# Optimization experiments

Hardware: AMD Instinct MI355X
Metric: run time of the kernel (lower is better)

Reference implementation:

```python
import jax, jax.numpy as jnp
import numpy as np

V, D, B, L = 100000, 64, 4096, 200

def setup_inputs() -> dict:
    key = jax.random.key(0)
    ks = jax.random.split(key, 10)
    s = 0.05  # keep activations in a sane range for sigmoid
    return {
        "item_ids": jax.random.randint(ks[0], (B,), 0, V),
        "history": jax.random.randint(ks[1], (B, L), 0, V),
        "hist_len": jax.random.randint(ks[2], (B,), 1, L + 1),
        "emb_table": jax.random.normal(ks[3], (V, D), jnp.float32) * s,
        "aW1": jax.random.normal(ks[4], (3 * D, D), jnp.float32) * s,
        "ab1": jnp.zeros((D,), jnp.float32),
        "aW2": jax.random.normal(ks[5], (D, 1), jnp.float32) * s,
        "ab2": jnp.zeros((1,), jnp.float32),
        "fW1": jax.random.normal(ks[6], (3 * D, 128), jnp.float32) * s,
        "fb1": jnp.zeros((128,), jnp.float32),
        "fW2": jax.random.normal(ks[7], (128, 64), jnp.float32) * s,
        "fb2": jnp.zeros((64,), jnp.float32),
        "fW3": jax.random.normal(ks[8], (64, 1), jnp.float32) * s,
        "fb3": jnp.zeros((1,), jnp.float32),
    }

def reference(item_ids, history, hist_len, emb_table, aW1, ab1, aW2, ab2,
              fW1, fb1, fW2, fb2, fW3, fb3):
    target = emb_table[item_ids]                      # [B, D]
    hist = emb_table[history]                         # [B, L, D]
    # original pads short histories with zero rows -> zero the padded tail
    mask = (jnp.arange(hist.shape[1])[None, :] < hist_len[:, None]).astype(hist.dtype)
    hist = hist * mask[..., None]
    tgt = jnp.broadcast_to(target[:, None, :], hist.shape)     # [B, L, D]
    # attention_fc takes 3*D features: (hist, target, hist*target)
    feat = jnp.concatenate([hist, tgt, hist * tgt], axis=-1)   # [B, L, 3D]
    h = jax.nn.relu(feat @ aW1 + ab1)                 # [B, L, D]
    scores = (h @ aW2 + ab2)[..., 0]                  # [B, L]
    # faithful to original: softmax over full padded length (no length mask)
    w = jax.nn.softmax(scores, axis=1)
    pooled = jnp.einsum('bl,bld->bd', w, hist)        # [B, D]
    comb = jnp.concatenate([target, pooled, pooled - target], axis=-1)  # [B, 3D]
    z = jax.nn.relu(comb @ fW1 + fb1)
    z = jax.nn.relu(z @ fW2 + fb2)
    return jax.nn.sigmoid(z @ fW3 + fb3)              # [B, 1]
```

## Files before the change

### kernel.cpp

```cpp
#include <hip/hip_runtime.h>
#include <hip/hip_bf16.h>

#define NV 100000
#define ND 64
#define NB 4096
#define NL 200
#define MT 13

typedef __bf16 bf16_t;
typedef __bf16 bf16x8 __attribute__((ext_vector_type(8)));
typedef __bf16 bf16x4 __attribute__((ext_vector_type(4)));
typedef float f32x4 __attribute__((ext_vector_type(4)));

#define TB_ELEMS ((long)NV * ND)
#define TBV (TB_ELEMS / 8)
#define FT1 (128 * 192)
#define FT2 (64 * 128)
#define AWB (192 * 64)
#define CVT_TASKS (TBV + FT1 + FT2 + AWB)

__global__ __launch_bounds__(256)
void cvt_kernel(const float* __restrict__ emb,
                const float* __restrict__ aW1,
                const float* __restrict__ fW1,
                const float* __restrict__ fW2,
                bf16_t* __restrict__ tb,
                bf16_t* __restrict__ fW1T,
                bf16_t* __restrict__ fW2T,
                bf16_t* __restrict__ awB)
{
    long t = (long)blockIdx.x * 256 + threadIdx.x;
    if (t >= CVT_TASKS) return;
    if (t < TBV) {
        long i = t * 8;
        f32x4 a0 = *(const f32x4*)(emb + i);
        f32x4 a1 = *(const f32x4*)(emb + i + 4);
        bf16x8 o;
#pragma unroll
        for (int j = 0; j < 4; ++j) { o[j] = (bf16_t)a0[j]; o[j + 4] = (bf16_t)a1[j]; }
        *(bf16x8*)(tb + i) = o;
    } else {
        int u = (int)(t - TBV);
        if (u < FT1) {
            int n = u / 192, k = u - n * 192;
            fW1T[u] = (bf16_t)fW1[k * 128 + n];
        } else if (u < FT1 + FT2) {
            int u2 = u - FT1;
            int n = u2 >> 7, k = u2 & 127;
            fW2T[u2] = (bf16_t)fW2[k * 64 + n];
        } else {
            int u3 = u - FT1 - FT2;
            awB[u3] = (bf16_t)aW1[u3];
        }
    }
}

__global__ __launch_bounds__(512, 4)
void din_kernel1(const int* __restrict__ item_ids,
                 const int* __restrict__ history,
                 const int* __restrict__ hist_len,
                 const float* __restrict__ emb,
                 const bf16_t* __restrict__ tb,
                 const float* __restrict__ aW1,
                 const bf16_t* __restrict__ awB,
                 const float* __restrict__ ab1,
                 const float* __restrict__ aW2,
                 const bf16_t* __restrict__ fW1T, const float* __restrict__ fb1,
                 const bf16_t* __restrict__ fW2T, const float* __restrict__ fb2,
                 const float* __restrict__ fW3, const float* __restrict__ fb3,
                 float* __restrict__ out)
{
    __shared__ __align__(16) bf16_t histA[2][208 * 64];
    __shared__ __align__(16) bf16_t wbT[2][64 * 64];
    __shared__ float tgt[2][64];
    __shared__ __align__(16) float scores[2][208];
    __shared__ float wts[2][208];
    __shared__ float pp2[2][256];
    __shared__ float red[2][8];
    __shared__ float cb2[2][64];

    bf16_t* comb16 = (bf16_t*)wbT;
    bf16_t* z1s    = (bf16_t*)wbT + 3200;
    float*  z2f    = (float*)((bf16_t*)wbT + 5376);

    const int b0  = blockIdx.x * 2;
    const int tid = threadIdx.x;
    const int len0 = hist_len[b0];
    const int len1 = hist_len[b0 + 1];

    if (tid < 128) {
        int bx = tid >> 6, d = tid & 63;
        tgt[bx][d] = emb[(long)item_ids[b0 + bx] * ND + d];
    }

    {
        const int p = tid & 1;
        const int s = tid >> 1;
        const int bxA = (s >= 208);
        const int lA  = s - bxA * 208;
        const int lB  = s + 48;
        const int lenA = bxA ? len1 : len0;
        const bool vB = (s < 160);
        const bf16x8 z = (bf16x8)(bf16_t)0.f;
        bf16x8 a0 = z, a1 = z, a2 = z, a3 = z;
        bf16x8 c0 = z, c1 = z, c2 = z, c3 = z;
        if (lA < lenA) {
            const bf16_t* src = tb + (long)history[(long)(b0 + bxA) * NL + lA] * ND + p * 32;
            a0 = *(const bf16x8*)(src);
            a1 = *(const bf16x8*)(src + 8);
            a2 = *(const bf16x8*)(src + 16);
            a3 = *(const bf16x8*)(src + 24);
        }
        if (vB && lB < len1) {
            const bf16_t* src = tb + (long)history[(long)(b0 + 1) * NL + lB] * ND + p * 32;
            c0 = *(const bf16x8*)(src);
            c1 = *(const bf16x8*)(src + 8);
            c2 = *(const bf16x8*)(src + 16);
            c3 = *(const bf16x8*)(src + 24);
        }
        {
            bf16_t* d = &histA[bxA][lA * 64];
            const int S = (lA & 7) << 3;
            *(bf16x8*)&d[(p * 32 +  0) ^ S] = a0;
            *(bf16x8*)&d[(p * 32 +  8) ^ S] = a1;
            *(bf16x8*)&d[(p * 32 + 16) ^ S] = a2;
            *(bf16x8*)&d[(p * 32 + 24) ^ S] = a3;
        }
        if (vB) {
            bf16_t* d = &histA[1][lB * 64];
            const int S = (lB & 7) << 3;
            *(bf16x8*)&d[(p * 32 +  0) ^ S] = c0;
            *(bf16x8*)&d[(p * 32 +  8) ^ S] = c1;
            *(bf16x8*)&d[(p * 32 + 16) ^ S] = c2;
            *(bf16x8*)&d[(p * 32 + 24) ^ S] = c3;
        }
    }

    {
        const int lane = tid & 63;
        const int w    = tid >> 6;
        const int bx   = w & 1;
        const int n    = ((w >> 1) << 4) | (lane & 15);
        const int kq   = lane >> 4;
        const long t0  = (long)item_ids[b0 + bx] * ND;
        f32x4 tka = *(const f32x4*)(emb + t0 + kq * 16);
        f32x4 tkb = *(const f32x4*)(emb + t0 + kq * 16 + 4);
        f32x4 tkc = *(const f32x4*)(emb + t0 + kq * 16 + 8);
        f32x4 tkd = *(const f32x4*)(emb + t0 + kq * 16 + 12);
        float csum = 0.f;
        bf16x8 w0v, w1v;
#pragma unroll
        for (int i = 0; i < 16; ++i) {
            int k = kq * 16 + i;
            float tk = (i < 4) ? tka[i] : (i < 8) ? tkb[i - 4]
                     : (i < 12) ? tkc[i - 8] : tkd[i - 12];
            float ah = (float)awB[k * 64 + n];
            float am = aW1[(64 + k) * 64 + n];
            float ap = (float)awB[(128 + k) * 64 + n];
            float wv = ah + tk * ap;
            if (i < 8) w0v[i] = (bf16_t)wv; else w1v[i - 8] = (bf16_t)wv;
            csum += tk * am;
        }
        const int S = (n & 7) << 3;
        *(bf16x8*)&wbT[bx][n * 64 + ((kq * 16    ) ^ S)] = w0v;
        *(bf16x8*)&wbT[bx][n * 64 + ((kq * 16 + 8) ^ S)] = w1v;
        csum += __shfl_xor(csum, 16, 64);
        csum += __shfl_xor(csum, 32, 64);
        if (kq == 0) cb2[bx][n] = ab1[n] + csum;
    }
    __syncthreads();

    {
        const int wave = tid >> 6;
        const int lane = tid & 63;
        const int bx   = wave & 1;
        const int col  = lane & 15;
        const int quad = lane >> 4;

        bf16x8 afrag[4][2];
#pragma unroll
        for (int nt = 0; nt < 4; ++nt) {
            const int n = nt * 16 + col;
            const int S = (n & 7) << 3;
#pragma unroll
            for (int kb = 0; kb < 2; ++kb)
                afrag[nt][kb] = *(const bf16x8*)&wbT[bx][n * 64 + ((kb * 32 + quad * 8) ^ S)];
        }
        float cv[4][4], a2[4][4];
#pragma unroll
        for (int nt = 0; nt < 4; ++nt)
#pragma unroll
            for (int i = 0; i < 4; ++i) {
                const int no = nt * 16 + quad * 4 + i;
                cv[nt][i] = cb2[bx][no];
                a2[nt][i] = aW2[no];
            }

        for (int mt = (wave >> 1); mt < MT; mt += 4) {
            const int l = mt * 16 + col;
            const int S = (l & 7) << 3;
            const bf16_t* base = &histA[bx][l * 64];
            bf16x8 bf0 = *(const bf16x8*)&base[(     quad * 8) ^ S];
            bf16x8 bf1 = *(const bf16x8*)&base[(32 + quad * 8) ^ S];
            float sc = 0.f;
#pragma unroll
            for (int nt = 0; nt < 4; ++nt) {
                f32x4 acc = {cv[nt][0], cv[nt][1], cv[nt][2], cv[nt][3]};
                acc = __builtin_amdgcn_mfma_f32_16x16x32_bf16(afrag[nt][0], bf0, acc, 0, 0, 0);
                acc = __builtin_amdgcn_mfma_f32_16x16x32_bf16(afrag[nt][1], bf1, acc, 0, 0, 0);
#pragma unroll
                for (int i = 0; i < 4; ++i) {
                    float h = acc[i] > 0.f ? acc[i] : 0.f;
                    sc += h * a2[nt][i];
                }
            }
            sc += __shfl_xor(sc, 16, 64);
            sc += __shfl_xor(sc, 32, 64);
            if (quad == 0) scores[bx][mt * 16 + col] = sc;
        }
    }
    __syncthreads();

    {
        const int bx = tid >> 8, t = tid & 255;
        float s = (t < NL) ? scores[bx][t] : -1e30f;
        float m = s;
        for (int off = 32; off > 0; off >>= 1) m = fmaxf(m, __shfl_xor(m, off, 64));
        float e = (t < NL) ? __expf(s - m) : 0.f;
        if (t < NL) wts[bx][t] = e;
        else if (t < 208) wts[bx][t] = 0.f;
        float ss = e;
        for (int off = 32; off > 0; off >>= 1) ss += __shfl_xor(ss, off, 64);
        if ((t & 63) == 0) { red[bx][t >> 6] = m; red[bx][4 + (t >> 6)] = ss; }
    }
    __syncthreads();

    bf16x8 bw1[6]; float b1v;
    bf16x8 bw2[4]; float b2v = 0.f;
    {
        const int wave = tid >> 6, lane = tid & 63;
        const int col = lane & 15, quad = lane >> 4;
        const int n = wave * 16 + col;
#pragma unroll
        for (int ks = 0; ks < 6; ++ks)
            bw1[ks] = *(const bf16x8*)&fW1T[(long)n * 192 + ks * 32 + quad * 8];
        b1v = fb1[n];
        if (wave < 4) {
            const int n2 = wave * 16 + col;
#pragma unroll
            for (int ks = 0; ks < 4; ++ks)
                bw2[ks] = *(const bf16x8*)&fW2T[(long)n2 * 128 + ks * 32 + quad * 8];
            b2v = fb2[n2];
        }
    }

    {
        const int bx = tid >> 8, t = tid & 255;
        const int c = t & 15;
        const int g = t >> 4;
        const int w4 = (tid >> 6) & 3;
        const float m0 = red[bx][0], m1 = red[bx][1], m2 = red[bx][2], m3 = red[bx][3];
        const float mg = fmaxf(fmaxf(m0, m1), fmaxf(m2, m3));
        float sc0 = __expf(m0 - mg), sc1 = __expf(m1 - mg);
        float sc2 = __expf(m2 - mg), sc3 = __expf(m3 - mg);
        const float rtot = 1.f / (sc0 * red[bx][4] + sc1 * red[bx][5] +
                                  sc2 * red[bx][6] + sc3 * red[bx][7]);
        sc0 *= rtot; sc1 *= rtot; sc2 *= rtot; sc3 *= rtot;
        f32x4 acc = {0.f, 0.f, 0.f, 0.f};
#pragma unroll
        for (int j = 0; j < 13; ++j) {
            const int l = g + j * 16;
            const float scj = (j < 4) ? sc0 : (j < 8) ? sc1 : (j < 12) ? sc2 : sc3;
            const float wl = wts[bx][l] * scj;
            bf16x4 v = *(const bf16x4*)&histA[bx][l * 64 + ((c * 4) ^ ((l & 7) << 3))];
#pragma unroll
            for (int k = 0; k < 4; ++k) acc[k] += wl * (float)v[k];
        }
#pragma unroll
        for (int k = 0; k < 4; ++k) {
            acc[k] += __shfl_xor(acc[k], 16, 64);
            acc[k] += __shfl_xor(acc[k], 32, 64);
        }
        if ((tid & 63) < 16) *(f32x4*)&pp2[bx][w4 * 64 + c * 4] = acc;
    }
    __syncthreads();

    {
        const int bx = tid >> 8, t = tid & 255;
        if (t < 192) {
            const int d = t & 63;
            float v;
            if (t < 64) v = tgt[bx][d];
            else {
                float pl = pp2[bx][d] + pp2[bx][64 + d] + pp2[bx][128 + d] + pp2[bx][192 + d];
                v = (t < 128) ? pl : pl - tgt[bx][d];
            }
            comb16[bx * 200 + t] = (bf16_t)v;
        }
    }
    __syncthreads();

    {
        const int wave = tid >> 6, lane = tid & 63;
        const int col = lane & 15, quad = lane >> 4;
        f32x4 acc = {b1v, b1v, b1v, b1v};
#pragma unroll
        for (int ks = 0; ks < 6; ++ks) {
            bf16x8 a = *(const bf16x8*)&comb16[col * 200 + ks * 32 + quad * 8];
            acc = __builtin_amdgcn_mfma_f32_16x16x32_bf16(a, bw1[ks], acc, 0, 0, 0);
        }
        const int n = wave * 16 + col;
#pragma unroll
        for (int i = 0; i < 4; ++i) {
            const int m = quad * 4 + i;
            if (m < 2) z1s[m * 136 + n] = (bf16_t)fmaxf(acc[i], 0.f);
        }
    }
    __syncthreads();

    {
        const int wave = tid >> 6, lane = tid & 63;
        const int col = lane & 15, quad = lane >> 4;
        if (wave < 4) {
            f32x4 acc = {b2v, b2v, b2v, b2v};
#pragma unroll
            for (int ks = 0; ks < 4; ++ks) {
                bf16x8 a = *(const bf16x8*)&z1s[col * 136 + ks * 32 + quad * 8];
                acc = __builtin_amdgcn_mfma_f32_16x16x32_bf16(a, bw2[ks], acc, 0, 0, 0);
            }
            const int n2 = wave * 16 + col;
#pragma unroll
            for (int i = 0; i < 4; ++i) {
                const int m = quad * 4 + i;
                if (m < 2) z2f[m * 64 + n2] = fmaxf(acc[i], 0.f);
            }
        }
    }
    __syncthreads();

    if (tid < 128) {
        const int bx = tid >> 6, j = tid & 63;
        float s = z2f[bx * 64 + j] * fW3[j];
        for (int off = 32; off > 0; off >>= 1) s += __shfl_xor(s, off, 64);
        if (j == 0) out[b0 + bx] = 1.f / (1.f + __expf(-(s + fb3[0])));
    }
}

extern "C" void kernel_launch(void* const* d_in, const int* in_sizes, int n_in,
                              void* d_out, int out_size, void* d_ws, size_t ws_size,
                              hipStream_t stream) {
    const int*   item_ids = (const int*)d_in[0];
    const int*   history  = (const int*)d_in[1];
    const int*   hist_len = (const int*)d_in[2];
    const float* emb      = (const float*)d_in[3];
    const float* aW1      = (const float*)d_in[4];
    const float* ab1      = (const float*)d_in[5];
    const float* aW2      = (const float*)d_in[6];
    const float* fW1      = (const float*)d_in[8];
    const float* fb1      = (const float*)d_in[9];
    const float* fW2      = (const float*)d_in[10];
    const float* fb2      = (const float*)d_in[11];
    const float* fW3      = (const float*)d_in[12];
    const float* fb3      = (const float*)d_in[13];

    bf16_t* tb   = (bf16_t*)d_ws;
    bf16_t* fW1T = tb + TB_ELEMS;
    bf16_t* fW2T = fW1T + FT1;
    bf16_t* awBp = fW2T + FT2;

    cvt_kernel<<<(int)((CVT_TASKS + 255) / 256), 256, 0, stream>>>(
        emb, aW1, fW1, fW2, tb, fW1T, fW2T, awBp);
    din_kernel1<<<NB / 2, 512, 0, stream>>>(item_ids, history, hist_len, emb, tb,
                                            aW1, awBp, ab1, aW2,
                                            fW1T, fb1, fW2T, fb2, fW3, fb3,
                                            (float*)d_out);
}
```

Baseline: 141.8 us.

## Make DIN kernel persistent with register-prefetched next-pair history gather

The main kernel now launches a fixed grid of 512 blocks. Each block loops over four batch pairs and issues the history-row gathers for the next pair into registers while it runs the softmax and pooling of the current one. The FC weight fragments are loaded once per block instead of once per pair. The bf16 copy of aW1 is dropped and the fp32 aW1 is read directly. This hides gather latency behind compute at the cost of higher register pressure, fewer resident blocks, and one extra barrier per iteration.

```diff
diff --git a/kernel.cpp b/kernel.cpp
--- a/kernel.cpp
+++ b/kernel.cpp
@@ -6,6 +6,8 @@
 #define NB 4096
 #define NL 200
 #define MT 13
+#define GRID 512
+#define NIT 4
 
 typedef __bf16 bf16_t;
 typedef __bf16 bf16x8 __attribute__((ext_vector_type(8)));
@@ -16,18 +18,15 @@
 #define TBV (TB_ELEMS / 8)
 #define FT1 (128 * 192)
 #define FT2 (64 * 128)
-#define AWB (192 * 64)
-#define CVT_TASKS (TBV + FT1 + FT2 + AWB)
+#define CVT_TASKS (TBV + FT1 + FT2)
 
 __global__ __launch_bounds__(256)
 void cvt_kernel(const float* __restrict__ emb,
-                const float* __restrict__ aW1,
                 const float* __restrict__ fW1,
                 const float* __restrict__ fW2,
                 bf16_t* __restrict__ tb,
                 bf16_t* __restrict__ fW1T,
-                bf16_t* __restrict__ fW2T,
-                bf16_t* __restrict__ awB)
+                bf16_t* __restrict__ fW2T)
 {
     long t = (long)blockIdx.x * 256 + threadIdx.x;
     if (t >= CVT_TASKS) return;
@@ -44,13 +43,10 @@
         if (u < FT1) {
             int n = u / 192, k = u - n * 192;
             fW1T[u] = (bf16_t)fW1[k * 128 + n];
-        } else if (u < FT1 + FT2) {
+        } else {
             int u2 = u - FT1;
             int n = u2 >> 7, k = u2 & 127;
             fW2T[u2] = (bf16_t)fW2[k * 64 + n];
-        } else {
-            int u3 = u - FT1 - FT2;
-            awB[u3] = (bf16_t)aW1[u3];
         }
     }
 }
@@ -62,7 +58,6 @@
                  const float* __restrict__ emb,
                  const bf16_t* __restrict__ tb,
                  const float* __restrict__ aW1,
-                 const bf16_t* __restrict__ awB,
                  const float* __restrict__ ab1,
                  const float* __restrict__ aW2,
                  const bf16_t* __restrict__ fW1T, const float* __restrict__ fb1,
@@ -83,40 +78,59 @@
     bf16_t* z1s    = (bf16_t*)wbT + 3200;
     float*  z2f    = (float*)((bf16_t*)wbT + 5376);
 
-    const int b0  = blockIdx.x * 2;
+    const int bid = blockIdx.x;
     const int tid = threadIdx.x;
-    const int len0 = hist_len[b0];
-    const int len1 = hist_len[b0 + 1];
-
-    if (tid < 128) {
-        int bx = tid >> 6, d = tid & 63;
-        tgt[bx][d] = emb[(long)item_ids[b0 + bx] * ND + d];
+
+    const int p    = tid & 1;
+    const int s    = tid >> 1;
+    const int bxA  = (s >= 208);
+    const int lA   = s - bxA * 208;
+    const int lB   = s + 48;
+    const bool hasB = (s < 160);
+
+    const int wave = tid >> 6, lane = tid & 63;
+    const int col  = lane & 15, quad = lane >> 4;
+
+    bf16x8 bw1[6]; float b1v;
+    bf16x8 bw2[4]; float b2v = 0.f;
+    {
+        const int n = wave * 16 + col;
+#pragma unroll
+        for (int ks = 0; ks < 6; ++ks)
+            bw1[ks] = *(const bf16x8*)&fW1T[(long)n * 192 + ks * 32 + quad * 8];
+        b1v = fb1[n];
+        if (wave < 4) {
+            const int n2 = wave * 16 + col;
+#pragma unroll
+            for (int ks = 0; ks < 4; ++ks)
+                bw2[ks] = *(const bf16x8*)&fW2T[(long)n2 * 128 + ks * 32 + quad * 8];
+            b2v = fb2[n2];
+        }
     }
 
+    const bf16x8 z8 = (bf16x8)(bf16_t)0.f;
+
+    int  pr = bid;
+    long it0, it1;
     {
-        const int p = tid & 1;
-        const int s = tid >> 1;
-        const int bxA = (s >= 208);
-        const int lA  = s - bxA * 208;
-        const int lB  = s + 48;
+        const int b0 = pr * 2;
+        it0 = (long)item_ids[b0] * ND;
+        it1 = (long)item_ids[b0 + 1] * ND;
+        const int len0 = hist_len[b0], len1 = hist_len[b0 + 1];
+        float tg = 0.f;
+        if (tid < 128) tg = emb[((tid >> 6) ? it1 : it0) + (tid & 63)];
         const int lenA = bxA ? len1 : len0;
-        const bool vB = (s < 160);
-        const bf16x8 z = (bf16x8)(bf16_t)0.f;
-        bf16x8 a0 = z, a1 = z, a2 = z, a3 = z;
-        bf16x8 c0 = z, c1 = z, c2 = z, c3 = z;
+        bf16x8 a0 = z8, a1 = z8, a2 = z8, a3 = z8;
+        bf16x8 c0 = z8, c1 = z8, c2 = z8, c3 = z8;
         if (lA < lenA) {
             const bf16_t* src = tb + (long)history[(long)(b0 + bxA) * NL + lA] * ND + p * 32;
-            a0 = *(const bf16x8*)(src);
-            a1 = *(const bf16x8*)(src + 8);
-            a2 = *(const bf16x8*)(src + 16);
-            a3 = *(const bf16x8*)(src + 24);
-        }
-        if (vB && lB < len1) {
+            a0 = *(const bf16x8*)(src);      a1 = *(const bf16x8*)(src + 8);
+            a2 = *(const bf16x8*)(src + 16); a3 = *(const bf16x8*)(src + 24);
+        }
+        if (hasB && lB < len1) {
             const bf16_t* src = tb + (long)history[(long)(b0 + 1) * NL + lB] * ND + p * 32;
-            c0 = *(const bf16x8*)(src);
-            c1 = *(const bf16x8*)(src + 8);
-            c2 = *(const bf16x8*)(src + 16);
-            c3 = *(const bf16x8*)(src + 24);
+            c0 = *(const bf16x8*)(src);      c1 = *(const bf16x8*)(src + 8);
+            c2 = *(const bf16x8*)(src + 16); c3 = *(const bf16x8*)(src + 24);
         }
         {
             bf16_t* d = &histA[bxA][lA * 64];
@@ -126,7 +140,7 @@
             *(bf16x8*)&d[(p * 32 + 16) ^ S] = a2;
             *(bf16x8*)&d[(p * 32 + 24) ^ S] = a3;
         }
-        if (vB) {
+        if (hasB) {
             bf16_t* d = &histA[1][lB * 64];
             const int S = (lB & 7) << 3;
             *(bf16x8*)&d[(p * 32 +  0) ^ S] = c0;
@@ -134,193 +148,197 @@
             *(bf16x8*)&d[(p * 32 + 16) ^ S] = c2;
             *(bf16x8*)&d[(p * 32 + 24) ^ S] = c3;
         }
+        if (tid < 128) tgt[tid >> 6][tid & 63] = tg;
     }
 
-    {
-        const int lane = tid & 63;
-        const int w    = tid >> 6;
-        const int bx   = w & 1;
-        const int n    = ((w >> 1) << 4) | (lane & 15);
-        const int kq   = lane >> 4;
-        const long t0  = (long)item_ids[b0 + bx] * ND;
-        f32x4 tka = *(const f32x4*)(emb + t0 + kq * 16);
-        f32x4 tkb = *(const f32x4*)(emb + t0 + kq * 16 + 4);
-        f32x4 tkc = *(const f32x4*)(emb + t0 + kq * 16 + 8);
-        f32x4 tkd = *(const f32x4*)(emb + t0 + kq * 16 + 12);
-        float csum = 0.f;
-        bf16x8 w0v, w1v;
-#pragma unroll
-        for (int i = 0; i < 16; ++i) {
-            int k = kq * 16 + i;
-            float tk = (i < 4) ? tka[i] : (i < 8) ? tkb[i - 4]
-                     : (i < 12) ? tkc[i - 8] : tkd[i - 12];
-            float ah = (float)awB[k * 64 + n];
-            float am = aW1[(64 + k) * 64 + n];
-            float ap = (float)awB[(128 + k) * 64 + n];
-            float wv = ah + tk * ap;
-            if (i < 8) w0v[i] = (bf16_t)wv; else w1v[i - 8] = (bf16_t)wv;
-            csum += tk * am;
-        }
-        const int S = (n & 7) << 3;
-        *(bf16x8*)&wbT[bx][n * 64 + ((kq * 16    ) ^ S)] = w0v;
-        *(bf16x8*)&wbT[bx][n * 64 + ((kq * 16 + 8) ^ S)] = w1v;
-        csum += __shfl_xor(csum, 16, 64);
-        csum += __shfl_xor(csum, 32, 64);
-        if (kq == 0) cb2[bx][n] = ab1[n] + csum;
-    }
-    __syncthreads();
-
-    {
-        const int wave = tid >> 6;
-        const int lane = tid & 63;
-        const int bx   = wave & 1;
-        const int col  = lane & 15;
-        const int quad = lane >> 4;
-
-        bf16x8 afrag[4][2];
-#pragma unroll
-        for (int nt = 0; nt < 4; ++nt) {
-            const int n = nt * 16 + col;
+    for (int it = 0; it < NIT; ++it) {
+        const int b0 = pr * 2;
+
+        {
+            const int bx = wave & 1;
+            const int n  = ((wave >> 1) << 4) | col;
+            const int kq = quad;
+            const long t0 = bx ? it1 : it0;
+            f32x4 tka = *(const f32x4*)(emb + t0 + kq * 16);
+            f32x4 tkb = *(const f32x4*)(emb + t0 + kq * 16 + 4);
+            f32x4 tkc = *(const f32x4*)(emb + t0 + kq * 16 + 8);
+            f32x4 tkd = *(const f32x4*)(emb + t0 + kq * 16 + 12);
+            float csum = 0.f;
+            bf16x8 w0v, w1v;
+#pragma unroll
+            for (int i = 0; i < 16; ++i) {
+                int k = kq * 16 + i;
+                float tk = (i < 4) ? tka[i] : (i < 8) ? tkb[i - 4]
+                         : (i < 12) ? tkc[i - 8] : tkd[i - 12];
+                float ah = aW1[k * 64 + n];
+                float am = aW1[(64 + k) * 64 + n];
+                float ap = aW1[(128 + k) * 64 + n];
+                float wv = ah + tk * ap;
+                if (i < 8) w0v[i] = (bf16_t)wv; else w1v[i - 8] = (bf16_t)wv;
+                csum += tk * am;
+            }
             const int S = (n & 7) << 3;
-#pragma unroll
-            for (int kb = 0; kb < 2; ++kb)
-                afrag[nt][kb] = *(const bf16x8*)&wbT[bx][n * 64 + ((kb * 32 + quad * 8) ^ S)];
-        }
-        float cv[4][4], a2[4][4];
-#pragma unroll
-        for (int nt = 0; nt < 4; ++nt)
+            *(bf16x8*)&wbT[bx][n * 64 + ((kq * 16    ) ^ S)] = w0v;
+            *(bf16x8*)&wbT[bx][n * 64 + ((kq * 16 + 8) ^ S)] = w1v;
+            csum += __shfl_xor(csum, 16, 64);
+            csum += __shfl_xor(csum, 32, 64);
+            if (kq == 0) cb2[bx][n] = ab1[n] + csum;
+        }
+        __syncthreads();
+
+        {
+            const int bx = wave & 1;
+            bf16x8 afrag[4][2];
+#pragma unroll
+            for (int nt = 0; nt < 4; ++nt) {
+                const int n = nt * 16 + col;
+                const int S = (n & 7) << 3;
+#pragma unroll
+                for (int kb = 0; kb < 2; ++kb)
+                    afrag[nt][kb] = *(const bf16x8*)&wbT[bx][n * 64 + ((kb * 32 + quad * 8) ^ S)];
+            }
+            float cv[4][4], a2[4][4];
+#pragma unroll
+            for (int nt = 0; nt < 4; ++nt)
+#pragma unroll
+                for (int i = 0; i < 4; ++i) {
+                    const int no = nt * 16 + quad * 4 + i;
+                    cv[nt][i] = cb2[bx][no];
+                    a2[nt][i] = aW2[no];
+                }
+            for (int mt = (wave >> 1); mt < MT; mt += 4) {
+                const int l = mt * 16 + col;
+                const int S = (l & 7) << 3;
+                const bf16_t* base = &histA[bx][l * 64];
+                bf16x8 bf0 = *(const bf16x8*)&base[(     quad * 8) ^ S];
+                bf16x8 bf1 = *(const bf16x8*)&base[(32 + quad * 8) ^ S];
+                float sc = 0.f;
+#pragma unroll
+                for (int nt = 0; nt < 4; ++nt) {
+                    f32x4 acc = {cv[nt][0], cv[nt][1], cv[nt][2], cv[nt][3]};
+                    acc = __builtin_amdgcn_mfma_f32_16x16x32_bf16(afrag[nt][0], bf0, acc, 0, 0, 0);
+                    acc = __builtin_amdgcn_mfma_f32_16x16x32_bf16(afrag[nt][1], bf1, acc, 0, 0, 0);
+#pragma unroll
+                    for (int i = 0; i < 4; ++i) {
+                        float h = acc[i] > 0.f ? acc[i] : 0.f;
+                        sc += h * a2[nt][i];
+                    }
+                }
+                sc += __shfl_xor(sc, 16, 64);
+                sc += __shfl_xor(sc, 32, 64);
+                if (quad == 0) scores[bx][mt * 16 + col] = sc;
+            }
+        }
+        __syncthreads();
+
+        const bool more = (it + 1 < NIT);
+        long nit0 = 0, nit1 = 0;
+        int  nlenA = 0, nlen1 = 0, idxA = 0, idxB = 0;
+        if (more) {
+            const int nb0 = (pr + GRID) * 2;
+            nit0 = (long)item_ids[nb0] * ND;
+            nit1 = (long)item_ids[nb0 + 1] * ND;
+            const int nl0 = hist_len[nb0];
+            nlen1 = hist_len[nb0 + 1];
+            nlenA = bxA ? nlen1 : nl0;
+            if (lA < NL) idxA = history[(long)(nb0 + bxA) * NL + lA];
+            if (hasB)    idxB = history[(long)(nb0 + 1) * NL + lB];
+        }
+        __builtin_amdgcn_sched_barrier(0);
+
+        {
+            const int bx = tid >> 8, t = tid & 255;
+            float sv = (t < NL) ? scores[bx][t] : -1e30f;
+            float m = sv;
+            for (int off = 32; off > 0; off >>= 1) m = fmaxf(m, __shfl_xor(m, off, 64));
+            float e = (t < NL) ? __expf(sv - m) : 0.f;
+            if (t < NL) wts[bx][t] = e;
+            else if (t < 208) wts[bx][t] = 0.f;
+            float ss = e;
+            for (int off = 32; off > 0; off >>= 1) ss += __shfl_xor(ss, off, 64);
+            if ((t & 63) == 0) { red[bx][t >> 6] = m; red[bx][4 + (t >> 6)] = ss; }
+        }
+        __syncthreads();
+
+        {
+            const int bx = tid >> 8, t = tid & 255;
+            const int c = t & 15, g = t >> 4;
+            const int w4 = (tid >> 6) & 3;
+            const float m0 = red[bx][0], m1 = red[bx][1], m2 = red[bx][2], m3 = red[bx][3];
+            const float mg = fmaxf(fmaxf(m0, m1), fmaxf(m2, m3));
+            float sc0 = __expf(m0 - mg), sc1 = __expf(m1 - mg);
+            float sc2 = __expf(m2 - mg), sc3 = __expf(m3 - mg);
+            const float rtot = 1.f / (sc0 * red[bx][4] + sc1 * red[bx][5] +
+                                      sc2 * red[bx][6] + sc3 * red[bx][7]);
+            sc0 *= rtot; sc1 *= rtot; sc2 *= rtot; sc3 *= rtot;
+            f32x4 acc = {0.f, 0.f, 0.f, 0.f};
+#pragma unroll
+            for (int j = 0; j < 13; ++j) {
+                const int l = g + j * 16;
+                const float scj = (j < 4) ? sc0 : (j < 8) ? sc1 : (j < 12) ? sc2 : sc3;
+                const float wl = wts[bx][l] * scj;
+                bf16x4 v = *(const bf16x4*)&histA[bx][l * 64 + ((c * 4) ^ ((l & 7) << 3))];
+#pragma unroll
+                for (int k = 0; k < 4; ++k) acc[k] += wl * (float)v[k];
+            }
+#pragma unroll
+            for (int k = 0; k < 4; ++k) {
+                acc[k] += __shfl_xor(acc[k], 16, 64);
+                acc[k] += __shfl_xor(acc[k], 32, 64);
+            }
+            if ((tid & 63) < 16) *(f32x4*)&pp2[bx][w4 * 64 + c * 4] = acc;
+        }
+
+        bf16x8 ra0 = z8, ra1 = z8, ra2 = z8, ra3 = z8;
+        bf16x8 rc0 = z8, rc1 = z8, rc2 = z8, rc3 = z8;
+        float ntg = 0.f;
+        if (more) {
+            if (lA < nlenA) {
+                const bf16_t* src = tb + (long)idxA * ND + p * 32;
+                ra0 = *(const bf16x8*)(src);      ra1 = *(const bf16x8*)(src + 8);
+                ra2 = *(const bf16x8*)(src + 16); ra3 = *(const bf16x8*)(src + 24);
+            }
+            if (hasB && lB < nlen1) {
+                const bf16_t* src = tb + (long)idxB * ND + p * 32;
+                rc0 = *(const bf16x8*)(src);      rc1 = *(const bf16x8*)(src + 8);
+                rc2 = *(const bf16x8*)(src + 16); rc3 = *(const bf16x8*)(src + 24);
+            }
+            if (tid < 128) ntg = emb[((tid >> 6) ? nit1 : nit0) + (tid & 63)];
+        }
+        __builtin_amdgcn_sched_barrier(0);
+        __syncthreads();
+
+        {
+            const int bx = tid >> 8, t = tid & 255;
+            if (t < 192) {
+                const int d = t & 63;
+                float v;
+                if (t < 64) v = tgt[bx][d];
+                else {
+                    float pl = pp2[bx][d] + pp2[bx][64 + d] + pp2[bx][128 + d] + pp2[bx][192 + d];
+                    v = (t < 128) ? pl : pl - tgt[bx][d];
+                }
+                comb16[bx * 200 + t] = (bf16_t)v;
+            }
+        }
+        __syncthreads();
+
+        {
+            f32x4 acc = {b1v, b1v, b1v, b1v};
+#pragma unroll
+            for (int ks = 0; ks < 6; ++ks) {
+                bf16x8 a = *(const bf16x8*)&comb16[col * 200 + ks * 32 + quad * 8];
+                acc = __builtin_amdgcn_mfma_f32_16x16x32_bf16(a, bw1[ks], acc, 0, 0, 0);
+            }
+            const int n = wave * 16 + col;
 #pragma unroll
             for (int i = 0; i < 4; ++i) {
-                const int no = nt * 16 + quad * 4 + i;
-                cv[nt][i] = cb2[bx][no];
-                a2[nt][i] = aW2[no];
-            }
-
-        for (int mt = (wave >> 1); mt < MT; mt += 4) {
-            const int l = mt * 16 + col;
-            const int S = (l & 7) << 3;
-            const bf16_t* base = &histA[bx][l * 64];
-            bf16x8 bf0 = *(const bf16x8*)&base[(     quad * 8) ^ S];
-            bf16x8 bf1 = *(const bf16x8*)&base[(32 + quad * 8) ^ S];
-            float sc = 0.f;
-#pragma unroll
-            for (int nt = 0; nt < 4; ++nt) {
-                f32x4 acc = {cv[nt][0], cv[nt][1], cv[nt][2], cv[nt][3]};
-                acc = __builtin_amdgcn_mfma_f32_16x16x32_bf16(afrag[nt][0], bf0, acc, 0, 0, 0);
-                acc = __builtin_amdgcn_mfma_f32_16x16x32_bf16(afrag[nt][1], bf1, acc, 0, 0, 0);
-#pragma unroll
-                for (int i = 0; i < 4; ++i) {
-                    float h = acc[i] > 0.f ? acc[i] : 0.f;
-                    sc += h * a2[nt][i];
-                }
-            }
-            sc += __shfl_xor(sc, 16, 64);
-            sc += __shfl_xor(sc, 32, 64);
-            if (quad == 0) scores[bx][mt * 16 + col] = sc;
-        }
-    }
-    __syncthreads();
-
-    {
-        const int bx = tid >> 8, t = tid & 255;
-        float s = (t < NL) ? scores[bx][t] : -1e30f;
-        float m = s;
-        for (int off = 32; off > 0; off >>= 1) m = fmaxf(m, __shfl_xor(m, off, 64));
-        float e = (t < NL) ? __expf(s - m) : 0.f;
-        if (t < NL) wts[bx][t] = e;
-        else if (t < 208) wts[bx][t] = 0.f;
-        float ss = e;
-        for (int off = 32; off > 0; off >>= 1) ss += __shfl_xor(ss, off, 64);
-        if ((t & 63) == 0) { red[bx][t >> 6] = m; red[bx][4 + (t >> 6)] = ss; }
-    }
-    __syncthreads();
-
-    bf16x8 bw1[6]; float b1v;
-    bf16x8 bw2[4]; float b2v = 0.f;
-    {
-        const int wave = tid >> 6, lane = tid & 63;
-        const int col = lane & 15, quad = lane >> 4;
-        const int n = wave * 16 + col;
-#pragma unroll
-        for (int ks = 0; ks < 6; ++ks)
-            bw1[ks] = *(const bf16x8*)&fW1T[(long)n * 192 + ks * 32 + quad * 8];
-        b1v = fb1[n];
-        if (wave < 4) {
-            const int n2 = wave * 16 + col;
-#pragma unroll
-            for (int ks = 0; ks < 4; ++ks)
-                bw2[ks] = *(const bf16x8*)&fW2T[(long)n2 * 128 + ks * 32 + quad * 8];
-            b2v = fb2[n2];
-        }
-    }
-
-    {
-        const int bx = tid >> 8, t = tid & 255;
-        const int c = t & 15;
-        const int g = t >> 4;
-        const int w4 = (tid >> 6) & 3;
-        const float m0 = red[bx][0], m1 = red[bx][1], m2 = red[bx][2], m3 = red[bx][3];
-        const float mg = fmaxf(fmaxf(m0, m1), fmaxf(m2, m3));
-        float sc0 = __expf(m0 - mg), sc1 = __expf(m1 - mg);
-        float sc2 = __expf(m2 - mg), sc3 = __expf(m3 - mg);
-        const float rtot = 1.f / (sc0 * red[bx][4] + sc1 * red[bx][5] +
-                                  sc2 * red[bx][6] + sc3 * red[bx][7]);
-        sc0 *= rtot; sc1 *= rtot; sc2 *= rtot; sc3 *= rtot;
-        f32x4 acc = {0.f, 0.f, 0.f, 0.f};
-#pragma unroll
-        for (int j = 0; j < 13; ++j) {
-            const int l = g + j * 16;
-            const float scj = (j < 4) ? sc0 : (j < 8) ? sc1 : (j < 12) ? sc2 : sc3;
-            const float wl = wts[bx][l] * scj;
-            bf16x4 v = *(const bf16x4*)&histA[bx][l * 64 + ((c * 4) ^ ((l & 7) << 3))];
-#pragma unroll
-            for (int k = 0; k < 4; ++k) acc[k] += wl * (float)v[k];
-        }
-#pragma unroll
-        for (int k = 0; k < 4; ++k) {
-            acc[k] += __shfl_xor(acc[k], 16, 64);
-            acc[k] += __shfl_xor(acc[k], 32, 64);
-        }
-        if ((tid & 63) < 16) *(f32x4*)&pp2[bx][w4 * 64 + c * 4] = acc;
-    }
-    __syncthreads();
-
-    {
-        const int bx = tid >> 8, t = tid & 255;
-        if (t < 192) {
-            const int d = t & 63;
-            float v;
-            if (t < 64) v = tgt[bx][d];
-            else {
-                float pl = pp2[bx][d] + pp2[bx][64 + d] + pp2[bx][128 + d] + pp2[bx][192 + d];
-                v = (t < 128) ? pl : pl - tgt[bx][d];
-            }
-            comb16[bx * 200 + t] = (bf16_t)v;
-        }
-    }
-    __syncthreads();
-
-    {
-        const int wave = tid >> 6, lane = tid & 63;
-        const int col = lane & 15, quad = lane >> 4;
-        f32x4 acc = {b1v, b1v, b1v, b1v};
-#pragma unroll
-        for (int ks = 0; ks < 6; ++ks) {
-            bf16x8 a = *(const bf16x8*)&comb16[col * 200 + ks * 32 + quad * 8];
-            acc = __builtin_amdgcn_mfma_f32_16x16x32_bf16(a, bw1[ks], acc, 0, 0, 0);
-        }
-        const int n = wave * 16 + col;
-#pragma unroll
-        for (int i = 0; i < 4; ++i) {
-            const int m = quad * 4 + i;
-            if (m < 2) z1s[m * 136 + n] = (bf16_t)fmaxf(acc[i], 0.f);
-        }
-    }
-    __syncthreads();
-
-    {
-        const int wave = tid >> 6, lane = tid & 63;
-        const int col = lane & 15, quad = lane >> 4;
+                const int m = quad * 4 + i;
+                if (m < 2) z1s[m * 136 + n] = (bf16_t)fmaxf(acc[i], 0.f);
+            }
+        }
+        __syncthreads();
+
         if (wave < 4) {
             f32x4 acc = {b2v, b2v, b2v, b2v};
 #pragma unroll
@@ -335,14 +353,37 @@
                 if (m < 2) z2f[m * 64 + n2] = fmaxf(acc[i], 0.f);
             }
         }
-    }
-    __syncthreads();
-
-    if (tid < 128) {
-        const int bx = tid >> 6, j = tid & 63;
-        float s = z2f[bx * 64 + j] * fW3[j];
-        for (int off = 32; off > 0; off >>= 1) s += __shfl_xor(s, off, 64);
-        if (j == 0) out[b0 + bx] = 1.f / (1.f + __expf(-(s + fb3[0])));
+        __syncthreads();
+
+        if (tid < 128) {
+            const int bx = tid >> 6, j = tid & 63;
+            float sv = z2f[bx * 64 + j] * fW3[j];
+            for (int off = 32; off > 0; off >>= 1) sv += __shfl_xor(sv, off, 64);
+            if (j == 0) out[b0 + bx] = 1.f / (1.f + __expf(-(sv + fb3[0])));
+        }
+
+        if (more) {
+            {
+                bf16_t* d = &histA[bxA][lA * 64];
+                const int S = (lA & 7) << 3;
+                *(bf16x8*)&d[(p * 32 +  0) ^ S] = ra0;
+                *(bf16x8*)&d[(p * 32 +  8) ^ S] = ra1;
+                *(bf16x8*)&d[(p * 32 + 16) ^ S] = ra2;
+                *(bf16x8*)&d[(p * 32 + 24) ^ S] = ra3;
+            }
+            if (hasB) {
+                bf16_t* d = &histA[1][lB * 64];
+                const int S = (lB & 7) << 3;
+                *(bf16x8*)&d[(p * 32 +  0) ^ S] = rc0;
+                *(bf16x8*)&d[(p * 32 +  8) ^ S] = rc1;
+                *(bf16x8*)&d[(p * 32 + 16) ^ S] = rc2;
+                *(bf16x8*)&d[(p * 32 + 24) ^ S] = rc3;
+            }
+            if (tid < 128) tgt[tid >> 6][tid & 63] = ntg;
+            it0 = nit0; it1 = nit1;
+        }
+        pr += GRID;
+        __syncthreads();
     }
 }
 
@@ -366,12 +407,11 @@
     bf16_t* tb   = (bf16_t*)d_ws;
     bf16_t* fW1T = tb + TB_ELEMS;
     bf16_t* fW2T = fW1T + FT1;
-    bf16_t* awBp = fW2T + FT2;
-
-    cvt_kernel<<<(int)((CVT_TASKS + 255) / 256), 256, 0, stream>>>(
-        emb, aW1, fW1, fW2, tb, fW1T, fW2T, awBp);
-    din_kernel1<<<NB / 2, 512, 0, stream>>>(item_ids, history, hist_len, emb, tb,
-                                            aW1, awBp, ab1, aW2,
-                                            fW1T, fb1, fW2T, fb2, fW3, fb3,
-                                            (float*)d_out);
+
+    cvt_kernel<<<(int)((CVT_TASKS + 255) / 256), 256, 0, stream>>>(emb, fW1, fW2,
+                                                                   tb, fW1T, fW2T);
+    din_kernel1<<<GRID, 512, 0, stream>>>(item_ids, history, hist_len, emb, tb,
+                                          aW1, ab1, aW2,
+                                          fW1T, fb1, fW2T, fb2, fW3, fb3,
+                                          (float*)d_out);
 }
```

New measurement: 235.6 us. +66.2%, slower.

## Gather history rows directly into LDS via global_load_lds with zero page

Applied to the files above, without the earlier changes.

Replaces the register-staged history gather with direct global-to-LDS loads (global_load_lds, 16 bytes per lane), keeping the XOR swizzle by permuting the source column instead of the destination. Padded rows read from a small zeroed page in workspace so every lane issues a uniform load. The bf16 copy of aW1 is dropped and the fp32 aW1 is read directly when folding the target into the attention weights. The aim is to cut VGPR pressure and instruction count in the gather, but it depends on the LDS write layout of global_load_lds matching the swizzled indexing used downstream.

```diff
diff --git a/kernel.cpp b/kernel.cpp
--- a/kernel.cpp
+++ b/kernel.cpp
@@ -16,18 +16,17 @@
 #define TBV (TB_ELEMS / 8)
 #define FT1 (128 * 192)
 #define FT2 (64 * 128)
-#define AWB (192 * 64)
-#define CVT_TASKS (TBV + FT1 + FT2 + AWB)
+#define ZPV 64
+#define CVT_TASKS (TBV + FT1 + FT2 + ZPV)
 
 __global__ __launch_bounds__(256)
 void cvt_kernel(const float* __restrict__ emb,
-                const float* __restrict__ aW1,
                 const float* __restrict__ fW1,
                 const float* __restrict__ fW2,
                 bf16_t* __restrict__ tb,
                 bf16_t* __restrict__ fW1T,
                 bf16_t* __restrict__ fW2T,
-                bf16_t* __restrict__ awB)
+                bf16_t* __restrict__ zpage)
 {
     long t = (long)blockIdx.x * 256 + threadIdx.x;
     if (t >= CVT_TASKS) return;
@@ -50,7 +49,7 @@
             fW2T[u2] = (bf16_t)fW2[k * 64 + n];
         } else {
             int u3 = u - FT1 - FT2;
-            awB[u3] = (bf16_t)aW1[u3];
+            *(bf16x8*)(zpage + u3 * 8) = (bf16x8)(bf16_t)0.f;
         }
     }
 }
@@ -61,8 +60,8 @@
                  const int* __restrict__ hist_len,
                  const float* __restrict__ emb,
                  const bf16_t* __restrict__ tb,
+                 const bf16_t* __restrict__ zpage,
                  const float* __restrict__ aW1,
-                 const bf16_t* __restrict__ awB,
                  const float* __restrict__ ab1,
                  const float* __restrict__ aW2,
                  const bf16_t* __restrict__ fW1T, const float* __restrict__ fb1,
@@ -88,61 +87,46 @@
     const int len0 = hist_len[b0];
     const int len1 = hist_len[b0 + 1];
 
+    const int wave = tid >> 6, lane = tid & 63;
+    const int col  = lane & 15, quad = lane >> 4;
+
     if (tid < 128) {
         int bx = tid >> 6, d = tid & 63;
         tgt[bx][d] = emb[(long)item_ids[b0 + bx] * ND + d];
     }
 
     {
-        const int p = tid & 1;
-        const int s = tid >> 1;
-        const int bxA = (s >= 208);
-        const int lA  = s - bxA * 208;
-        const int lB  = s + 48;
-        const int lenA = bxA ? len1 : len0;
-        const bool vB = (s < 160);
-        const bf16x8 z = (bf16x8)(bf16_t)0.f;
-        bf16x8 a0 = z, a1 = z, a2 = z, a3 = z;
-        bf16x8 c0 = z, c1 = z, c2 = z, c3 = z;
-        if (lA < lenA) {
-            const bf16_t* src = tb + (long)history[(long)(b0 + bxA) * NL + lA] * ND + p * 32;
-            a0 = *(const bf16x8*)(src);
-            a1 = *(const bf16x8*)(src + 8);
-            a2 = *(const bf16x8*)(src + 16);
-            a3 = *(const bf16x8*)(src + 24);
-        }
-        if (vB && lB < len1) {
-            const bf16_t* src = tb + (long)history[(long)(b0 + 1) * NL + lB] * ND + p * 32;
-            c0 = *(const bf16x8*)(src);
-            c1 = *(const bf16x8*)(src + 8);
-            c2 = *(const bf16x8*)(src + 16);
-            c3 = *(const bf16x8*)(src + 24);
-        }
-        {
-            bf16_t* d = &histA[bxA][lA * 64];
-            const int S = (lA & 7) << 3;
-            *(bf16x8*)&d[(p * 32 +  0) ^ S] = a0;
-            *(bf16x8*)&d[(p * 32 +  8) ^ S] = a1;
-            *(bf16x8*)&d[(p * 32 + 16) ^ S] = a2;
-            *(bf16x8*)&d[(p * 32 + 24) ^ S] = a3;
-        }
-        if (vB) {
-            bf16_t* d = &histA[1][lB * 64];
-            const int S = (lB & 7) << 3;
-            *(bf16x8*)&d[(p * 32 +  0) ^ S] = c0;
-            *(bf16x8*)&d[(p * 32 +  8) ^ S] = c1;
-            *(bf16x8*)&d[(p * 32 + 16) ^ S] = c2;
-            *(bf16x8*)&d[(p * 32 + 24) ^ S] = c3;
-        }
-    }
-
-    {
-        const int lane = tid & 63;
-        const int w    = tid >> 6;
-        const int bx   = w & 1;
-        const int n    = ((w >> 1) << 4) | (lane & 15);
-        const int kq   = lane >> 4;
-        const long t0  = (long)item_ids[b0 + bx] * ND;
+        const int r = lane >> 3;
+        const int c = lane & 7;
+#pragma unroll
+        for (int j = 0; j < 7; ++j) {
+            const int R = wave * 52 + j * 8;
+            const int nrows = (j == 6) ? 4 : 8;
+            const int l  = R + r;
+            const int bx = (l >= 208);
+            const int lr = l - (bx ? 208 : 0);
+            const int lenx = bx ? len1 : len0;
+            const bf16_t* gsrc;
+            if (lr < lenx) {
+                int idx = history[(long)(b0 + bx) * NL + lr];
+                gsrc = tb + (long)idx * ND + ((c ^ (lr & 7)) * 8);
+            } else {
+                gsrc = zpage + c * 8;
+            }
+            if (r < nrows) {
+                __builtin_amdgcn_global_load_lds(
+                    (const __attribute__((address_space(1))) void*)gsrc,
+                    (__attribute__((address_space(3))) void*)(&histA[0][0] + (long)R * 64),
+                    16, 0, 0);
+            }
+        }
+    }
+
+    {
+        const int bx = wave & 1;
+        const int n  = ((wave >> 1) << 4) | col;
+        const int kq = quad;
+        const long t0 = (long)item_ids[b0 + bx] * ND;
         f32x4 tka = *(const f32x4*)(emb + t0 + kq * 16);
         f32x4 tkb = *(const f32x4*)(emb + t0 + kq * 16 + 4);
         f32x4 tkc = *(const f32x4*)(emb + t0 + kq * 16 + 8);
@@ -154,9 +138,9 @@
             int k = kq * 16 + i;
             float tk = (i < 4) ? tka[i] : (i < 8) ? tkb[i - 4]
                      : (i < 12) ? tkc[i - 8] : tkd[i - 12];
-            float ah = (float)awB[k * 64 + n];
+            float ah = aW1[k * 64 + n];
             float am = aW1[(64 + k) * 64 + n];
-            float ap = (float)awB[(128 + k) * 64 + n];
+            float ap = aW1[(128 + k) * 64 + n];
             float wv = ah + tk * ap;
             if (i < 8) w0v[i] = (bf16_t)wv; else w1v[i - 8] = (bf16_t)wv;
             csum += tk * am;
@@ -171,12 +155,7 @@
     __syncthreads();
 
     {
-        const int wave = tid >> 6;
-        const int lane = tid & 63;
-        const int bx   = wave & 1;
-        const int col  = lane & 15;
-        const int quad = lane >> 4;
-
+        const int bx = wave & 1;
         bf16x8 afrag[4][2];
 #pragma unroll
         for (int nt = 0; nt < 4; ++nt) {
@@ -238,8 +217,6 @@
     bf16x8 bw1[6]; float b1v;
     bf16x8 bw2[4]; float b2v = 0.f;
     {
-        const int wave = tid >> 6, lane = tid & 63;
-        const int col = lane & 15, quad = lane >> 4;
         const int n = wave * 16 + col;
 #pragma unroll
         for (int ks = 0; ks < 6; ++ks)
@@ -301,8 +278,6 @@
     __syncthreads();
 
     {
-        const int wave = tid >> 6, lane = tid & 63;
-        const int col = lane & 15, quad = lane >> 4;
         f32x4 acc = {b1v, b1v, b1v, b1v};
 #pragma unroll
         for (int ks = 0; ks < 6; ++ks) {
@@ -319,8 +294,6 @@
     __syncthreads();
 
     {
-        const int wave = tid >> 6, lane = tid & 63;
-        const int col = lane & 15, quad = lane >> 4;
         if (wave < 4) {
             f32x4 acc = {b2v, b2v, b2v, b2v};
 #pragma unroll
@@ -363,15 +336,15 @@
     const float* fW3      = (const float*)d_in[12];
     const float* fb3      = (const float*)d_in[13];
 
-    bf16_t* tb   = (bf16_t*)d_ws;
-    bf16_t* fW1T = tb + TB_ELEMS;
-    bf16_t* fW2T = fW1T + FT1;
-    bf16_t* awBp = fW2T + FT2;
+    bf16_t* tb    = (bf16_t*)d_ws;
+    bf16_t* fW1T  = tb + TB_ELEMS;
+    bf16_t* fW2T  = fW1T + FT1;
+    bf16_t* zpage = fW2T + FT2;
 
     cvt_kernel<<<(int)((CVT_TASKS + 255) / 256), 256, 0, stream>>>(
-        emb, aW1, fW1, fW2, tb, fW1T, fW2T, awBp);
+        emb, fW1, fW2, tb, fW1T, fW2T, zpage);
     din_kernel1<<<NB / 2, 512, 0, stream>>>(item_ids, history, hist_len, emb, tb,
-                                            aW1, awBp, ab1, aW2,
+                                            zpage, aW1, ab1, aW2,
                                             fW1T, fb1, fW2T, fb2, fW3, fb3,
                                             (float*)d_out);
 }
```

Result: slower. 145.1 us (+2.4%).
